# Performance work log

Measured on AMD Instinct MI355X. Metric: run time of the kernel, lower is better.

The kernel has to match this reference:

```python
import jax, jax.numpy as jnp
import numpy as np

HIDDEN = 2048
N_HEADS = 16
HEAD_DIM = HIDDEN // N_HEADS
MAX_POS = 4096
ROPE_THETA = 10000.0
B, S = 2, 4096


def rotate_half(x):
    d = x.shape[-1] // 2
    return jnp.concatenate([-x[..., d:], x[..., :d]], axis=-1)


def make_rope_cache(seq_len, dim, base):
    inv_freq = 1.0 / (base ** (np.arange(0, dim, 2, dtype=np.float32) / dim))
    t = np.arange(seq_len, dtype=np.float32)
    freqs = np.einsum('i,j->ij', t, inv_freq)
    emb = np.concatenate([freqs, freqs], axis=-1)
    return jnp.asarray(np.cos(emb)), jnp.asarray(np.sin(emb))


def setup_inputs() -> dict:
    key = jax.random.key(0)
    k1, k2, k3, k4, k5, k6 = jax.random.split(key, 6)
    hidden_states = jax.random.normal(k1, (B, S, HIDDEN), dtype=jnp.float32)
    # causal additive mask [B,1,S,S]
    causal = jnp.where(jnp.tril(jnp.ones((S, S), dtype=bool)), 0.0, -1e9).astype(jnp.float32)
    attention_mask = jnp.broadcast_to(causal[None, None], (B, 1, S, S))
    position_ids = jnp.broadcast_to(jnp.arange(S, dtype=jnp.int64)[None], (B, S))
    scale = 0.02
    Wq = jax.random.normal(k2, (HIDDEN, HIDDEN), dtype=jnp.float32) * scale
    Wk = jax.random.normal(k3, (HIDDEN, HIDDEN), dtype=jnp.float32) * scale
    Wv = jax.random.normal(k4, (HIDDEN, HIDDEN), dtype=jnp.float32) * scale
    Wo = jax.random.normal(k5, (HIDDEN, HIDDEN), dtype=jnp.float32) * scale
    return {"hidden_states": hidden_states, "attention_mask": attention_mask,
            "position_ids": position_ids, "Wq": Wq, "Wk": Wk, "Wv": Wv, "Wo": Wo}


def reference(hidden_states, attention_mask, position_ids, Wq, Wk, Wv, Wo):
    bsz, q_len, _ = hidden_states.shape
    # projections (torch Linear: x @ W.T; here W stored as [in,out] -> x @ W)
    q = (hidden_states @ Wq).reshape(bsz, q_len, N_HEADS, HEAD_DIM).transpose(0, 2, 1, 3)
    k = (hidden_states @ Wk).reshape(bsz, q_len, N_HEADS, HEAD_DIM).transpose(0, 2, 1, 3)
    v = (hidden_states @ Wv).reshape(bsz, q_len, N_HEADS, HEAD_DIM).transpose(0, 2, 1, 3)
    cos_c, sin_c = make_rope_cache(q_len, HEAD_DIM, ROPE_THETA)
    cos = cos_c[position_ids][:, None]  # [B,1,S,Dh]
    sin = sin_c[position_ids][:, None]
    q = q * cos + rotate_half(q) * sin
    k = k * cos + rotate_half(k) * sin
    scores = jnp.einsum('bhqd,bhkd->bhqk', q, k) / jnp.sqrt(jnp.float32(HEAD_DIM))
    scores = scores + attention_mask
    probs = jax.nn.softmax(scores.astype(jnp.float32), axis=-1).astype(q.dtype)
    attn = jnp.einsum('bhqk,bhkd->bhqd', probs, v)
    attn = attn.transpose(0, 2, 1, 3).reshape(bsz, q_len, HIDDEN)
    return attn @ Wo
```

## Files before the change

### kernel.cpp

```cpp
#include <hip/hip_runtime.h>

#define HID 2048
#define NHEADS 16
#define DHEAD 128
#define BB 2
#define SS 4096
#define MTOT (BB * SS)

typedef __attribute__((ext_vector_type(8))) short short8;
typedef __attribute__((ext_vector_type(8))) unsigned short ushort8;
typedef __attribute__((ext_vector_type(4))) float floatx4;
typedef __attribute__((ext_vector_type(16))) float floatx16;

static __device__ __forceinline__ ushort f2bf(float f) {
  unsigned x = __float_as_uint(f);
  return (ushort)((x + 0x7fffu + ((x >> 16) & 1u)) >> 16);
}
static __device__ __forceinline__ float bf2f(ushort u) {
  return __uint_as_float(((unsigned)u) << 16);
}
static __device__ __forceinline__ unsigned cvtpk_bf16(float lo, float hi) {
  unsigned r;
  asm("v_cvt_pk_bf16_f32 %0, %1, %2" : "=v"(r) : "v"(lo), "v"(hi));
  return r;
}
static __device__ __forceinline__ void pl32swap(unsigned& a, unsigned& b) {
  asm volatile("v_permlane32_swap_b32 %0, %1" : "+v"(a), "+v"(b));
}
static __device__ __forceinline__ floatx16 fz16() {
  floatx16 z;
#pragma unroll
  for (int i = 0; i < 16; i++) z[i] = 0.f;
  return z;
}

#define GL16(g, l)                                                   \
  __builtin_amdgcn_global_load_lds(                                  \
      (const __attribute__((address_space(1))) unsigned int*)(g),    \
      (__attribute__((address_space(3))) unsigned int*)(l), 16, 0, 0)

__global__ __launch_bounds__(256) void k_prep(const float* __restrict__ X,
                                              ushort* __restrict__ Xb,
                                              const float* __restrict__ Wq,
                                              const float* __restrict__ Wk,
                                              const float* __restrict__ Wv,
                                              const float* __restrict__ Wo,
                                              ushort* __restrict__ Wqt,
                                              ushort* __restrict__ Wkt,
                                              ushort* __restrict__ Wvt,
                                              ushort* __restrict__ Wot,
                                              float* __restrict__ cosT,
                                              float* __restrict__ sinT) {
  __shared__ float tile[64][65];
  int id = blockIdx.x, t = threadIdx.x;
  if (id < 2048) {
    int i = id * 256 + t;
    const int n4 = MTOT * HID / 4, stride = 2048 * 256;
    for (; i < n4; i += stride) {
      float4 v = reinterpret_cast<const float4*>(X)[i];
      ushort4 u;
      u.x = f2bf(v.x); u.y = f2bf(v.y); u.z = f2bf(v.z); u.w = f2bf(v.w);
      reinterpret_cast<ushort4*>(Xb)[i] = u;
    }
  } else if (id < 6144) {
    int w = (id - 2048) >> 10;
    int bid = (id - 2048) & 1023;
    const float* W = (w == 0) ? Wq : (w == 1) ? Wk : (w == 2) ? Wv : Wo;
    ushort* Wt = (w == 0) ? Wqt : (w == 1) ? Wkt : (w == 2) ? Wvt : Wot;
    int n0 = (bid & 31) * 64, k0 = (bid >> 5) * 64;
#pragma unroll
    for (int i = 0; i < 16; i++) {
      int idx = t + i * 256, r = idx >> 6, c = idx & 63;
      tile[r][c] = W[(size_t)(k0 + r) * HID + n0 + c];
    }
    __syncthreads();
#pragma unroll
    for (int i = 0; i < 16; i++) {
      int idx = t + i * 256, r = idx >> 6, c = idx & 63;
      Wt[(size_t)(n0 + r) * HID + k0 + c] = f2bf(tile[c][r]);
    }
  } else {
    int idx = (id - 6144) * 256 + t;
    int pos = idx >> 6, j = idx & 63;
    float inv = powf(10000.0f, -(float)(2 * j) * (1.0f / 128.0f));
    float a = (float)pos * inv;
    cosT[idx] = cosf(a);
    sinT[idx] = sinf(a);
  }
}

__global__ void k_rope(ushort* __restrict__ Q, ushort* __restrict__ Kb,
                       const float* __restrict__ cosT, const float* __restrict__ sinT) {
  const float kSc = 0.12751742f;
  int idx = blockIdx.x * 256 + threadIdx.x;
  int j8 = (idx & 7) * 8;
  int hh = (idx >> 3) & (NHEADS - 1);
  int srow = idx >> 7;
  int pos = srow & (SS - 1);
  float4 c0 = *reinterpret_cast<const float4*>(&cosT[pos * 64 + j8]);
  float4 c1 = *reinterpret_cast<const float4*>(&cosT[pos * 64 + j8 + 4]);
  float4 s0 = *reinterpret_cast<const float4*>(&sinT[pos * 64 + j8]);
  float4 s1 = *reinterpret_cast<const float4*>(&sinT[pos * 64 + j8 + 4]);
  float cc[8] = {c0.x, c0.y, c0.z, c0.w, c1.x, c1.y, c1.z, c1.w};
  float ss[8] = {s0.x, s0.y, s0.z, s0.w, s1.x, s1.y, s1.z, s1.w};
  size_t base = (size_t)srow * HID + hh * DHEAD + j8;
  ushort8 qa = *reinterpret_cast<ushort8*>(&Q[base]);
  ushort8 qb = *reinterpret_cast<ushort8*>(&Q[base + 64]);
  ushort8 ka = *reinterpret_cast<ushort8*>(&Kb[base]);
  ushort8 kb = *reinterpret_cast<ushort8*>(&Kb[base + 64]);
  ushort8 o1, o2, o3, o4;
#pragma unroll
  for (int i = 0; i < 8; i++) {
    float a1 = bf2f(qa[i]), a2 = bf2f(qb[i]);
    o1[i] = f2bf((a1 * cc[i] - a2 * ss[i]) * kSc);
    o2[i] = f2bf((a2 * cc[i] + a1 * ss[i]) * kSc);
    float b1 = bf2f(ka[i]), b2 = bf2f(kb[i]);
    o3[i] = f2bf(b1 * cc[i] - b2 * ss[i]);
    o4[i] = f2bf(b2 * cc[i] + b1 * ss[i]);
  }
  *reinterpret_cast<ushort8*>(&Q[base]) = o1;
  *reinterpret_cast<ushort8*>(&Q[base + 64]) = o2;
  *reinterpret_cast<ushort8*>(&Kb[base]) = o3;
  *reinterpret_cast<ushort8*>(&Kb[base + 64]) = o4;
}

template <int OUT_BF16, int DUAL>
__global__ __launch_bounds__(512, 2) void k_gemm8(const ushort* __restrict__ A,
                                                  const ushort* __restrict__ Bt,
                                                  void* __restrict__ Cp,
                                                  const ushort* __restrict__ Bt2,
                                                  void* __restrict__ Cp2,
                                                  int Mr, int Nc, int Kd) {
  __shared__ ushort As[3][256 * 32];
  __shared__ ushort Bs[3][256 * 32];
  int t = threadIdx.x;
  int lane = t & 63, wid = t >> 6;
  int lrow = lane & 15, lk = lane >> 4;
  int wr = wid >> 2, wc = wid & 3;

  int id = blockIdx.x;
  if (DUAL && id >= 256) {
    Bt = Bt2;
    Cp = Cp2;
    id -= 256;
  }
  int nbx = Nc >> 8;
  int swz = (id & 7) * 32 + (id >> 3);
  int m0 = (swz / nbx) << 8, n0 = (swz % nbx) << 8;

  floatx4 acc[8][4];
#pragma unroll
  for (int i = 0; i < 8; i++)
#pragma unroll
    for (int j = 0; j < 4; j++) acc[i][j] = (floatx4){0.f, 0.f, 0.f, 0.f};

  int arow = t >> 2;
  int acol = (((t & 3) ^ (arow & 3)) << 3);
  const ushort* gA = A + (size_t)(m0 + arow) * Kd + acol;
  const ushort* gB = Bt + (size_t)(n0 + arow) * Kd + acol;

  auto STAGE = [&](int buf, int kt) {
    const ushort* a = gA + kt * 32;
    const ushort* bq = gB + kt * 32;
    GL16(a, (char*)As + buf * 16384 + t * 16);
    GL16(a + (size_t)128 * Kd, (char*)As + buf * 16384 + t * 16 + 8192);
    GL16(bq, (char*)Bs + buf * 16384 + t * 16);
    GL16(bq + (size_t)128 * Kd, (char*)Bs + buf * 16384 + t * 16 + 8192);
  };

  STAGE(0, 0);
  STAGE(1, 1);

  int nk = Kd >> 5;
  for (int tK = 0; tK < nk; ++tK) {
    if (tK + 1 < nk)
      asm volatile("s_waitcnt vmcnt(4)" ::: "memory");
    else
      asm volatile("s_waitcnt vmcnt(0)" ::: "memory");
    __builtin_amdgcn_s_barrier();
    asm volatile("" ::: "memory");
    int buf = tK % 3;
    const char* Ab_ = (const char*)As + buf * 16384;
    const char* Bb_ = (const char*)Bs + buf * 16384;
    short8 af[8], bfr[4];
#pragma unroll
    for (int fm = 0; fm < 8; fm++) {
      int row = wr * 128 + fm * 16 + lrow;
      af[fm] = *reinterpret_cast<const short8*>(
          Ab_ + ((row * 64 + lk * 16) ^ ((row & 3) << 4)));
    }
#pragma unroll
    for (int fn = 0; fn < 4; fn++) {
      int row = wc * 64 + fn * 16 + lrow;
      bfr[fn] = *reinterpret_cast<const short8*>(
          Bb_ + ((row * 64 + lk * 16) ^ ((row & 3) << 4)));
    }
    if (tK + 2 < nk) STAGE((tK + 2) % 3, tK + 2);
    __builtin_amdgcn_s_setprio(1);
#pragma unroll
    for (int fm = 0; fm < 8; fm++)
#pragma unroll
      for (int fn = 0; fn < 4; fn++)
        acc[fm][fn] = __builtin_amdgcn_mfma_f32_16x16x32_bf16(af[fm], bfr[fn],
                                                              acc[fm][fn], 0, 0, 0);
    __builtin_amdgcn_s_setprio(0);
  }

#pragma unroll
  for (int am = 0; am < 8; am++)
#pragma unroll
    for (int an = 0; an < 4; an++)
#pragma unroll
      for (int r = 0; r < 4; r++) {
        int m = m0 + wr * 128 + am * 16 + lk * 4 + r;
        int n = n0 + wc * 64 + an * 16 + lrow;
        if (OUT_BF16)
          ((ushort*)Cp)[(size_t)m * Nc + n] = f2bf(acc[am][an][r]);
        else
          ((float*)Cp)[(size_t)m * Nc + n] = acc[am][an][r];
      }
}

__global__ __launch_bounds__(512, 2) void k_fattn(const ushort* __restrict__ Qg,
                                                  const ushort* __restrict__ Kg,
                                                  const ushort* __restrict__ Vt2,
                                                  ushort* __restrict__ Og) {
  __shared__ ushort Ks[2][64 * 128];
  __shared__ ushort Vs[2][128 * 64];
  int t = threadIdx.x, lane = t & 63, wid = t >> 6;
  int l31 = lane & 31, hi = lane >> 5;
  int id = blockIdx.x;
  int qt = 15 - (id >> 5);
  int h = id & 15, b = (id >> 4) & 1;

  auto STAGE = [&](int buf, int kt) {
    int kv0 = kt * 64;
    const ushort* Kbase = Kg + (size_t)(b * SS + kv0) * HID + h * DHEAD;
    const ushort* Vbase = Vt2 + (size_t)(h * DHEAD) * MTOT + b * SS + kv0;
#pragma unroll
    for (int i = 0; i < 2; i++) {
      int L = t + i * 512;
      int row = L >> 4, cr = L & 15;
      GL16(Kbase + (size_t)row * HID + ((cr ^ (row & 15)) << 3),
           (char*)Ks + buf * 16384 + L * 16);
    }
#pragma unroll
    for (int i = 0; i < 2; i++) {
      int L = t + i * 512;
      int row = L >> 3, cr = L & 7;
      GL16(Vbase + (size_t)row * MTOT + ((cr ^ (row & 7)) << 3),
           (char*)Vs + buf * 16384 + L * 16);
    }
  };

  int q0 = qt * 256;
  int wq0 = q0 + wid * 32;
  int qlane = wq0 + l31;

  short8 qf[8];
  {
    const ushort* qb = Qg + (size_t)(b * SS + qlane) * HID + h * DHEAD + hi * 8;
#pragma unroll
    for (int ks = 0; ks < 8; ks++)
      qf[ks] = *reinterpret_cast<const short8*>(qb + ks * 16);
  }

  floatx16 accO[4];
#pragma unroll
  for (int db = 0; db < 4; db++) accO[db] = fz16();
  float mrow = -1e30f, lsum = 0.f;

  int nkt = (qt + 1) * 4;
  STAGE(0, 0);

  for (int kt = 0; kt < nkt; kt++) {
    int cur = kt & 1;
    int kv0 = kt * 64;
    bool pre = (kt + 1 < nkt);
    if (pre) {
      STAGE(cur ^ 1, kt + 1);
      asm volatile("s_waitcnt vmcnt(4)" ::: "memory");
    } else {
      asm volatile("s_waitcnt vmcnt(0)" ::: "memory");
    }
    __builtin_amdgcn_s_barrier();
    asm volatile("" ::: "memory");

    if (kv0 <= wq0 + 31) {
      const char* Kb_ = (const char*)Ks + cur * 16384;
      floatx16 accS[2];
      accS[0] = fz16(); accS[1] = fz16();
      __builtin_amdgcn_s_setprio(1);
#pragma unroll
      for (int ks = 0; ks < 8; ks++) {
#pragma unroll
        for (int kvb = 0; kvb < 2; kvb++) {
          int row = kvb * 32 + l31;
          int byte_ = (row * 256 + ks * 32 + hi * 16) ^ ((row & 15) << 4);
          short8 kf = *reinterpret_cast<const short8*>(Kb_ + byte_);
          accS[kvb] = __builtin_amdgcn_mfma_f32_32x32x16_bf16(kf, qf[ks], accS[kvb], 0, 0, 0);
        }
      }
      __builtin_amdgcn_s_setprio(0);

      if (kv0 + 63 > wq0) {
        int kvbase = kv0 + hi * 4;
#pragma unroll
        for (int kvb = 0; kvb < 2; kvb++)
#pragma unroll
          for (int r = 0; r < 16; r++) {
            int kvi = kvbase + kvb * 32 + (r & 3) + 8 * (r >> 2);
            if (kvi > qlane) accS[kvb][r] = -1e30f;
          }
      }

      float mA = -1e30f, mB = -1e30f, mC = -1e30f, mD = -1e30f;
#pragma unroll
      for (int r = 0; r < 16; r += 4) {
        mA = fmaxf(mA, fmaxf(accS[0][r], accS[1][r]));
        mB = fmaxf(mB, fmaxf(accS[0][r + 1], accS[1][r + 1]));
        mC = fmaxf(mC, fmaxf(accS[0][r + 2], accS[1][r + 2]));
        mD = fmaxf(mD, fmaxf(accS[0][r + 3], accS[1][r + 3]));
      }
      float mx = fmaxf(fmaxf(mA, mB), fmaxf(mC, mD));
      mx = fmaxf(mx, __shfl_xor(mx, 32));
      if (!__all(mx <= mrow + 8.0f)) {
        float mnew = fmaxf(mrow, mx);
        float corr = exp2f(mrow - mnew);
        mrow = mnew;
        lsum *= corr;
#pragma unroll
        for (int db = 0; db < 4; db++)
#pragma unroll
          for (int r = 0; r < 16; r++) accO[db][r] *= corr;
      }

      float sA = 0.f, sB = 0.f, sC = 0.f, sD = 0.f;
#pragma unroll
      for (int kvb = 0; kvb < 2; kvb++)
#pragma unroll
        for (int r = 0; r < 16; r += 4) {
          float p0 = exp2f(accS[kvb][r] - mrow);
          float p1 = exp2f(accS[kvb][r + 1] - mrow);
          float p2 = exp2f(accS[kvb][r + 2] - mrow);
          float p3 = exp2f(accS[kvb][r + 3] - mrow);
          accS[kvb][r] = p0; accS[kvb][r + 1] = p1;
          accS[kvb][r + 2] = p2; accS[kvb][r + 3] = p3;
          sA += p0; sB += p1; sC += p2; sD += p3;
        }
      lsum += ((sA + sB) + (sC + sD));

      const char* Vb_ = (const char*)Vs + cur * 16384;
#pragma unroll
      for (int ks = 0; ks < 4; ks++) {
        int kvb = ks >> 1, tt = ks & 1;
        unsigned w0 = cvtpk_bf16(accS[kvb][8 * tt + 0], accS[kvb][8 * tt + 1]);
        unsigned w2 = cvtpk_bf16(accS[kvb][8 * tt + 4], accS[kvb][8 * tt + 5]);
        pl32swap(w0, w2);
        unsigned w1 = cvtpk_bf16(accS[kvb][8 * tt + 2], accS[kvb][8 * tt + 3]);
        unsigned w3 = cvtpk_bf16(accS[kvb][8 * tt + 6], accS[kvb][8 * tt + 7]);
        pl32swap(w1, w3);
        union { unsigned u[4]; short8 v; } pf;
        pf.u[0] = w0; pf.u[1] = w1; pf.u[2] = w2; pf.u[3] = w3;
        __builtin_amdgcn_s_setprio(1);
#pragma unroll
        for (int db = 0; db < 4; db++) {
          int row = db * 32 + l31;
          int byte_ = (row * 128 + ks * 32 + hi * 16) ^ ((row & 7) << 4);
          short8 vf = *reinterpret_cast<const short8*>(Vb_ + byte_);
          accO[db] = __builtin_amdgcn_mfma_f32_32x32x16_bf16(vf, pf.v, accO[db], 0, 0, 0);
        }
        __builtin_amdgcn_s_setprio(0);
      }
    }
    asm volatile("" ::: "memory");
    __builtin_amdgcn_s_barrier();
    asm volatile("" ::: "memory");
  }

  float lt = lsum + __shfl_xor(lsum, 32);
  float inv = 1.0f / lt;
  char* sb = ((wid < 4) ? (char*)Ks : (char*)Vs) + (wid & 3) * 8192;
#pragma unroll
  for (int db = 0; db < 4; db++)
#pragma unroll
    for (int r = 0; r < 16; r += 2) {
      int d = db * 32 + (r & 3) + 8 * (r >> 2) + hi * 4;
      unsigned w = cvtpk_bf16(accO[db][r] * inv, accO[db][r + 1] * inv);
      int byte_ = (l31 * 256 + d * 2) ^ ((l31 & 15) << 4);
      *reinterpret_cast<unsigned*>(sb + byte_) = w;
    }
#pragma unroll
  for (int i = 0; i < 8; i++) {
    int row = i * 4 + (lane >> 4);
    int byte_ = (row * 256 + (lane & 15) * 16) ^ ((row & 15) << 4);
    ushort8 ov = *reinterpret_cast<const ushort8*>(sb + byte_);
    *reinterpret_cast<ushort8*>(Og + (size_t)(b * SS + wq0 + row) * HID + h * DHEAD +
                                (lane & 15) * 8) = ov;
  }
}

extern "C" void kernel_launch(void* const* d_in, const int* in_sizes, int n_in,
                              void* d_out, int out_size, void* d_ws, size_t ws_size,
                              hipStream_t stream) {
  const float* X = (const float*)d_in[0];
  const float* Wq = (const float*)d_in[3];
  const float* Wk = (const float*)d_in[4];
  const float* Wv = (const float*)d_in[5];
  const float* Wo = (const float*)d_in[6];
  float* out = (float*)d_out;

  char* p = (char*)d_ws;
  const size_t szXb = (size_t)MTOT * HID * 2;
  const size_t szW = (size_t)HID * HID * 2;
  ushort* Xb = (ushort*)p;  p += szXb;
  ushort* Wqt = (ushort*)p; p += szW;
  ushort* Wkt = (ushort*)p; p += szW;
  ushort* Wvt = (ushort*)p; p += szW;
  ushort* Wot = (ushort*)p; p += szW;
  ushort* Qb = (ushort*)p;  p += szXb;
  ushort* Kb = (ushort*)p;  p += szXb;
  ushort* Vt2 = (ushort*)p; p += szXb;
  ushort* Ab = (ushort*)p;  p += szXb;
  float* cosT = (float*)p;  p += (size_t)SS * 64 * 4;
  float* sinT = (float*)p;  p += (size_t)SS * 64 * 4;

  k_prep<<<7168, 256, 0, stream>>>(X, Xb, Wq, Wk, Wv, Wo, Wqt, Wkt, Wvt, Wot,
                                   cosT, sinT);

  k_gemm8<1, 1><<<512, 512, 0, stream>>>(Xb, Wqt, Qb, Wkt, Kb, MTOT, HID, HID);
  k_gemm8<1, 0><<<256, 512, 0, stream>>>(Wvt, Xb, Vt2, nullptr, nullptr, HID, MTOT, HID);

  k_rope<<<MTOT * NHEADS * 8 / 256, 256, 0, stream>>>(Qb, Kb, cosT, sinT);

  k_fattn<<<512, 512, 0, stream>>>(Qb, Kb, Vt2, Ab);

  k_gemm8<0, 0><<<256, 512, 0, stream>>>(Ab, Wot, out, nullptr, nullptr, MTOT, HID, HID);
}
```

Baseline: 518.4 us.

## Fuse RoPE into V-projection launch and retile flash attention to 128-query blocks

The separate RoPE kernel is folded into the V-projection GEMM launch as extra blocks, so the elementwise rotation runs alongside the GEMM instead of as its own launch. Flash attention is retiled from 256-query, 8-wave blocks with 64-key tiles to 128-query, 4-wave blocks with 32-key tiles. That doubles the grid and aims for better load balance across the causal triangle and higher occupancy. The trade-off is more barriers and staging steps per unit of work, less MFMA work per iteration, and RoPE blocks that carry the GEMM's large shared-memory footprint.

```diff
diff --git a/kernel.cpp b/kernel.cpp
--- a/kernel.cpp
+++ b/kernel.cpp
@@ -89,41 +89,6 @@
   }
 }
 
-__global__ void k_rope(ushort* __restrict__ Q, ushort* __restrict__ Kb,
-                       const float* __restrict__ cosT, const float* __restrict__ sinT) {
-  const float kSc = 0.12751742f;
-  int idx = blockIdx.x * 256 + threadIdx.x;
-  int j8 = (idx & 7) * 8;
-  int hh = (idx >> 3) & (NHEADS - 1);
-  int srow = idx >> 7;
-  int pos = srow & (SS - 1);
-  float4 c0 = *reinterpret_cast<const float4*>(&cosT[pos * 64 + j8]);
-  float4 c1 = *reinterpret_cast<const float4*>(&cosT[pos * 64 + j8 + 4]);
-  float4 s0 = *reinterpret_cast<const float4*>(&sinT[pos * 64 + j8]);
-  float4 s1 = *reinterpret_cast<const float4*>(&sinT[pos * 64 + j8 + 4]);
-  float cc[8] = {c0.x, c0.y, c0.z, c0.w, c1.x, c1.y, c1.z, c1.w};
-  float ss[8] = {s0.x, s0.y, s0.z, s0.w, s1.x, s1.y, s1.z, s1.w};
-  size_t base = (size_t)srow * HID + hh * DHEAD + j8;
-  ushort8 qa = *reinterpret_cast<ushort8*>(&Q[base]);
-  ushort8 qb = *reinterpret_cast<ushort8*>(&Q[base + 64]);
-  ushort8 ka = *reinterpret_cast<ushort8*>(&Kb[base]);
-  ushort8 kb = *reinterpret_cast<ushort8*>(&Kb[base + 64]);
-  ushort8 o1, o2, o3, o4;
-#pragma unroll
-  for (int i = 0; i < 8; i++) {
-    float a1 = bf2f(qa[i]), a2 = bf2f(qb[i]);
-    o1[i] = f2bf((a1 * cc[i] - a2 * ss[i]) * kSc);
-    o2[i] = f2bf((a2 * cc[i] + a1 * ss[i]) * kSc);
-    float b1 = bf2f(ka[i]), b2 = bf2f(kb[i]);
-    o3[i] = f2bf(b1 * cc[i] - b2 * ss[i]);
-    o4[i] = f2bf(b2 * cc[i] + b1 * ss[i]);
-  }
-  *reinterpret_cast<ushort8*>(&Q[base]) = o1;
-  *reinterpret_cast<ushort8*>(&Q[base + 64]) = o2;
-  *reinterpret_cast<ushort8*>(&Kb[base]) = o3;
-  *reinterpret_cast<ushort8*>(&Kb[base + 64]) = o4;
-}
-
 template <int OUT_BF16, int DUAL>
 __global__ __launch_bounds__(512, 2) void k_gemm8(const ushort* __restrict__ A,
                                                   const ushort* __restrict__ Bt,
@@ -221,39 +186,163 @@
       }
 }
 
-__global__ __launch_bounds__(512, 2) void k_fattn(const ushort* __restrict__ Qg,
+__global__ __launch_bounds__(512, 2) void k_gvrope(const ushort* __restrict__ A,
+                                                   const ushort* __restrict__ Bt,
+                                                   ushort* __restrict__ Cp,
+                                                   ushort* __restrict__ Q,
+                                                   ushort* __restrict__ Kb,
+                                                   const float* __restrict__ cosT,
+                                                   const float* __restrict__ sinT) {
+  __shared__ ushort As[3][256 * 32];
+  __shared__ ushort Bs[3][256 * 32];
+  int t = threadIdx.x;
+  if (blockIdx.x >= 256) {
+    const float kSc = 0.12751742f;
+    int idx = (blockIdx.x - 256) * 512 + t;
+    int j8 = (idx & 7) * 8;
+    int hh = (idx >> 3) & (NHEADS - 1);
+    int srow = idx >> 7;
+    int pos = srow & (SS - 1);
+    float4 c0 = *reinterpret_cast<const float4*>(&cosT[pos * 64 + j8]);
+    float4 c1 = *reinterpret_cast<const float4*>(&cosT[pos * 64 + j8 + 4]);
+    float4 s0 = *reinterpret_cast<const float4*>(&sinT[pos * 64 + j8]);
+    float4 s1 = *reinterpret_cast<const float4*>(&sinT[pos * 64 + j8 + 4]);
+    float cc[8] = {c0.x, c0.y, c0.z, c0.w, c1.x, c1.y, c1.z, c1.w};
+    float ss[8] = {s0.x, s0.y, s0.z, s0.w, s1.x, s1.y, s1.z, s1.w};
+    size_t base = (size_t)srow * HID + hh * DHEAD + j8;
+    ushort8 qa = *reinterpret_cast<ushort8*>(&Q[base]);
+    ushort8 qb = *reinterpret_cast<ushort8*>(&Q[base + 64]);
+    ushort8 ka = *reinterpret_cast<ushort8*>(&Kb[base]);
+    ushort8 kb = *reinterpret_cast<ushort8*>(&Kb[base + 64]);
+    ushort8 o1, o2, o3, o4;
+#pragma unroll
+    for (int i = 0; i < 8; i++) {
+      float a1 = bf2f(qa[i]), a2 = bf2f(qb[i]);
+      o1[i] = f2bf((a1 * cc[i] - a2 * ss[i]) * kSc);
+      o2[i] = f2bf((a2 * cc[i] + a1 * ss[i]) * kSc);
+      float b1 = bf2f(ka[i]), b2 = bf2f(kb[i]);
+      o3[i] = f2bf(b1 * cc[i] - b2 * ss[i]);
+      o4[i] = f2bf(b2 * cc[i] + b1 * ss[i]);
+    }
+    *reinterpret_cast<ushort8*>(&Q[base]) = o1;
+    *reinterpret_cast<ushort8*>(&Q[base + 64]) = o2;
+    *reinterpret_cast<ushort8*>(&Kb[base]) = o3;
+    *reinterpret_cast<ushort8*>(&Kb[base + 64]) = o4;
+    return;
+  }
+
+  const int Nc = MTOT, Kd = HID;
+  int lane = t & 63, wid = t >> 6;
+  int lrow = lane & 15, lk = lane >> 4;
+  int wr = wid >> 2, wc = wid & 3;
+  int id = blockIdx.x;
+  int nbx = Nc >> 8;
+  int swz = (id & 7) * 32 + (id >> 3);
+  int m0 = (swz / nbx) << 8, n0 = (swz % nbx) << 8;
+
+  floatx4 acc[8][4];
+#pragma unroll
+  for (int i = 0; i < 8; i++)
+#pragma unroll
+    for (int j = 0; j < 4; j++) acc[i][j] = (floatx4){0.f, 0.f, 0.f, 0.f};
+
+  int arow = t >> 2;
+  int acol = (((t & 3) ^ (arow & 3)) << 3);
+  const ushort* gA = A + (size_t)(m0 + arow) * Kd + acol;
+  const ushort* gB = Bt + (size_t)(n0 + arow) * Kd + acol;
+
+  auto STAGE = [&](int buf, int kt) {
+    const ushort* a = gA + kt * 32;
+    const ushort* bq = gB + kt * 32;
+    GL16(a, (char*)As + buf * 16384 + t * 16);
+    GL16(a + (size_t)128 * Kd, (char*)As + buf * 16384 + t * 16 + 8192);
+    GL16(bq, (char*)Bs + buf * 16384 + t * 16);
+    GL16(bq + (size_t)128 * Kd, (char*)Bs + buf * 16384 + t * 16 + 8192);
+  };
+
+  STAGE(0, 0);
+  STAGE(1, 1);
+
+  int nk = Kd >> 5;
+  for (int tK = 0; tK < nk; ++tK) {
+    if (tK + 1 < nk)
+      asm volatile("s_waitcnt vmcnt(4)" ::: "memory");
+    else
+      asm volatile("s_waitcnt vmcnt(0)" ::: "memory");
+    __builtin_amdgcn_s_barrier();
+    asm volatile("" ::: "memory");
+    int buf = tK % 3;
+    const char* Ab_ = (const char*)As + buf * 16384;
+    const char* Bb_ = (const char*)Bs + buf * 16384;
+    short8 af[8], bfr[4];
+#pragma unroll
+    for (int fm = 0; fm < 8; fm++) {
+      int row = wr * 128 + fm * 16 + lrow;
+      af[fm] = *reinterpret_cast<const short8*>(
+          Ab_ + ((row * 64 + lk * 16) ^ ((row & 3) << 4)));
+    }
+#pragma unroll
+    for (int fn = 0; fn < 4; fn++) {
+      int row = wc * 64 + fn * 16 + lrow;
+      bfr[fn] = *reinterpret_cast<const short8*>(
+          Bb_ + ((row * 64 + lk * 16) ^ ((row & 3) << 4)));
+    }
+    if (tK + 2 < nk) STAGE((tK + 2) % 3, tK + 2);
+    __builtin_amdgcn_s_setprio(1);
+#pragma unroll
+    for (int fm = 0; fm < 8; fm++)
+#pragma unroll
+      for (int fn = 0; fn < 4; fn++)
+        acc[fm][fn] = __builtin_amdgcn_mfma_f32_16x16x32_bf16(af[fm], bfr[fn],
+                                                              acc[fm][fn], 0, 0, 0);
+    __builtin_amdgcn_s_setprio(0);
+  }
+
+#pragma unroll
+  for (int am = 0; am < 8; am++)
+#pragma unroll
+    for (int an = 0; an < 4; an++)
+#pragma unroll
+      for (int r = 0; r < 4; r++) {
+        int m = m0 + wr * 128 + am * 16 + lk * 4 + r;
+        int n = n0 + wc * 64 + an * 16 + lrow;
+        Cp[(size_t)m * Nc + n] = f2bf(acc[am][an][r]);
+      }
+}
+
+__global__ __launch_bounds__(256, 4) void k_fattn(const ushort* __restrict__ Qg,
                                                   const ushort* __restrict__ Kg,
                                                   const ushort* __restrict__ Vt2,
                                                   ushort* __restrict__ Og) {
-  __shared__ ushort Ks[2][64 * 128];
-  __shared__ ushort Vs[2][128 * 64];
+  __shared__ ushort Ks[2][32 * 128];
+  __shared__ ushort Vs[2][128 * 32];
   int t = threadIdx.x, lane = t & 63, wid = t >> 6;
   int l31 = lane & 31, hi = lane >> 5;
   int id = blockIdx.x;
-  int qt = 15 - (id >> 5);
+  int qt = 31 - (id >> 5);
   int h = id & 15, b = (id >> 4) & 1;
 
   auto STAGE = [&](int buf, int kt) {
-    int kv0 = kt * 64;
+    int kv0 = kt * 32;
     const ushort* Kbase = Kg + (size_t)(b * SS + kv0) * HID + h * DHEAD;
     const ushort* Vbase = Vt2 + (size_t)(h * DHEAD) * MTOT + b * SS + kv0;
 #pragma unroll
     for (int i = 0; i < 2; i++) {
-      int L = t + i * 512;
+      int L = t + i * 256;
       int row = L >> 4, cr = L & 15;
       GL16(Kbase + (size_t)row * HID + ((cr ^ (row & 15)) << 3),
-           (char*)Ks + buf * 16384 + L * 16);
+           (char*)Ks + buf * 8192 + L * 16);
     }
 #pragma unroll
     for (int i = 0; i < 2; i++) {
-      int L = t + i * 512;
-      int row = L >> 3, cr = L & 7;
-      GL16(Vbase + (size_t)row * MTOT + ((cr ^ (row & 7)) << 3),
-           (char*)Vs + buf * 16384 + L * 16);
+      int L = t + i * 256;
+      int row = L >> 2, cr = L & 3;
+      GL16(Vbase + (size_t)row * MTOT + ((cr ^ (row & 3)) << 3),
+           (char*)Vs + buf * 8192 + L * 16);
     }
   };
 
-  int q0 = qt * 256;
+  int q0 = qt * 128;
   int wq0 = q0 + wid * 32;
   int qlane = wq0 + l31;
 
@@ -275,7 +364,7 @@
 
   for (int kt = 0; kt < nkt; kt++) {
     int cur = kt & 1;
-    int kv0 = kt * 64;
+    int kv0 = kt * 32;
     bool pre = (kt + 1 < nkt);
     if (pre) {
       STAGE(cur ^ 1, kt + 1);
@@ -287,40 +376,34 @@
     asm volatile("" ::: "memory");
 
     if (kv0 <= wq0 + 31) {
-      const char* Kb_ = (const char*)Ks + cur * 16384;
-      floatx16 accS[2];
-      accS[0] = fz16(); accS[1] = fz16();
+      const char* Kb_ = (const char*)Ks + cur * 8192;
+      floatx16 accS = fz16();
       __builtin_amdgcn_s_setprio(1);
 #pragma unroll
       for (int ks = 0; ks < 8; ks++) {
-#pragma unroll
-        for (int kvb = 0; kvb < 2; kvb++) {
-          int row = kvb * 32 + l31;
-          int byte_ = (row * 256 + ks * 32 + hi * 16) ^ ((row & 15) << 4);
-          short8 kf = *reinterpret_cast<const short8*>(Kb_ + byte_);
-          accS[kvb] = __builtin_amdgcn_mfma_f32_32x32x16_bf16(kf, qf[ks], accS[kvb], 0, 0, 0);
+        int row = l31;
+        int byte_ = (row * 256 + ks * 32 + hi * 16) ^ ((row & 15) << 4);
+        short8 kf = *reinterpret_cast<const short8*>(Kb_ + byte_);
+        accS = __builtin_amdgcn_mfma_f32_32x32x16_bf16(kf, qf[ks], accS, 0, 0, 0);
+      }
+      __builtin_amdgcn_s_setprio(0);
+
+      if (kv0 + 31 > wq0) {
+        int kvbase = kv0 + hi * 4;
+#pragma unroll
+        for (int r = 0; r < 16; r++) {
+          int kvi = kvbase + (r & 3) + 8 * (r >> 2);
+          if (kvi > qlane) accS[r] = -1e30f;
         }
       }
-      __builtin_amdgcn_s_setprio(0);
-
-      if (kv0 + 63 > wq0) {
-        int kvbase = kv0 + hi * 4;
-#pragma unroll
-        for (int kvb = 0; kvb < 2; kvb++)
-#pragma unroll
-          for (int r = 0; r < 16; r++) {
-            int kvi = kvbase + kvb * 32 + (r & 3) + 8 * (r >> 2);
-            if (kvi > qlane) accS[kvb][r] = -1e30f;
-          }
-      }
 
       float mA = -1e30f, mB = -1e30f, mC = -1e30f, mD = -1e30f;
 #pragma unroll
       for (int r = 0; r < 16; r += 4) {
-        mA = fmaxf(mA, fmaxf(accS[0][r], accS[1][r]));
-        mB = fmaxf(mB, fmaxf(accS[0][r + 1], accS[1][r + 1]));
-        mC = fmaxf(mC, fmaxf(accS[0][r + 2], accS[1][r + 2]));
-        mD = fmaxf(mD, fmaxf(accS[0][r + 3], accS[1][r + 3]));
+        mA = fmaxf(mA, accS[r]);
+        mB = fmaxf(mB, accS[r + 1]);
+        mC = fmaxf(mC, accS[r + 2]);
+        mD = fmaxf(mD, accS[r + 3]);
       }
       float mx = fmaxf(fmaxf(mA, mB), fmaxf(mC, mD));
       mx = fmaxf(mx, __shfl_xor(mx, 32));
@@ -337,28 +420,25 @@
 
       float sA = 0.f, sB = 0.f, sC = 0.f, sD = 0.f;
 #pragma unroll
-      for (int kvb = 0; kvb < 2; kvb++)
-#pragma unroll
-        for (int r = 0; r < 16; r += 4) {
-          float p0 = exp2f(accS[kvb][r] - mrow);
-          float p1 = exp2f(accS[kvb][r + 1] - mrow);
-          float p2 = exp2f(accS[kvb][r + 2] - mrow);
-          float p3 = exp2f(accS[kvb][r + 3] - mrow);
-          accS[kvb][r] = p0; accS[kvb][r + 1] = p1;
-          accS[kvb][r + 2] = p2; accS[kvb][r + 3] = p3;
-          sA += p0; sB += p1; sC += p2; sD += p3;
-        }
+      for (int r = 0; r < 16; r += 4) {
+        float p0 = exp2f(accS[r] - mrow);
+        float p1 = exp2f(accS[r + 1] - mrow);
+        float p2 = exp2f(accS[r + 2] - mrow);
+        float p3 = exp2f(accS[r + 3] - mrow);
+        accS[r] = p0; accS[r + 1] = p1; accS[r + 2] = p2; accS[r + 3] = p3;
+        sA += p0; sB += p1; sC += p2; sD += p3;
+      }
       lsum += ((sA + sB) + (sC + sD));
 
-      const char* Vb_ = (const char*)Vs + cur * 16384;
-#pragma unroll
-      for (int ks = 0; ks < 4; ks++) {
-        int kvb = ks >> 1, tt = ks & 1;
-        unsigned w0 = cvtpk_bf16(accS[kvb][8 * tt + 0], accS[kvb][8 * tt + 1]);
-        unsigned w2 = cvtpk_bf16(accS[kvb][8 * tt + 4], accS[kvb][8 * tt + 5]);
+      const char* Vb_ = (const char*)Vs + cur * 8192;
+#pragma unroll
+      for (int ks = 0; ks < 2; ks++) {
+        int tt = ks;
+        unsigned w0 = cvtpk_bf16(accS[8 * tt + 0], accS[8 * tt + 1]);
+        unsigned w2 = cvtpk_bf16(accS[8 * tt + 4], accS[8 * tt + 5]);
         pl32swap(w0, w2);
-        unsigned w1 = cvtpk_bf16(accS[kvb][8 * tt + 2], accS[kvb][8 * tt + 3]);
-        unsigned w3 = cvtpk_bf16(accS[kvb][8 * tt + 6], accS[kvb][8 * tt + 7]);
+        unsigned w1 = cvtpk_bf16(accS[8 * tt + 2], accS[8 * tt + 3]);
+        unsigned w3 = cvtpk_bf16(accS[8 * tt + 6], accS[8 * tt + 7]);
         pl32swap(w1, w3);
         union { unsigned u[4]; short8 v; } pf;
         pf.u[0] = w0; pf.u[1] = w1; pf.u[2] = w2; pf.u[3] = w3;
@@ -366,7 +446,7 @@
 #pragma unroll
         for (int db = 0; db < 4; db++) {
           int row = db * 32 + l31;
-          int byte_ = (row * 128 + ks * 32 + hi * 16) ^ ((row & 7) << 4);
+          int byte_ = (row * 64 + ks * 32 + hi * 16) ^ ((row & 3) << 4);
           short8 vf = *reinterpret_cast<const short8*>(Vb_ + byte_);
           accO[db] = __builtin_amdgcn_mfma_f32_32x32x16_bf16(vf, pf.v, accO[db], 0, 0, 0);
         }
@@ -380,7 +460,7 @@
 
   float lt = lsum + __shfl_xor(lsum, 32);
   float inv = 1.0f / lt;
-  char* sb = ((wid < 4) ? (char*)Ks : (char*)Vs) + (wid & 3) * 8192;
+  char* sb = ((wid < 2) ? (char*)Ks : (char*)Vs) + (wid & 1) * 8192;
 #pragma unroll
   for (int db = 0; db < 4; db++)
 #pragma unroll
@@ -429,11 +509,9 @@
                                    cosT, sinT);
 
   k_gemm8<1, 1><<<512, 512, 0, stream>>>(Xb, Wqt, Qb, Wkt, Kb, MTOT, HID, HID);
-  k_gemm8<1, 0><<<256, 512, 0, stream>>>(Wvt, Xb, Vt2, nullptr, nullptr, HID, MTOT, HID);
-
-  k_rope<<<MTOT * NHEADS * 8 / 256, 256, 0, stream>>>(Qb, Kb, cosT, sinT);
-
-  k_fattn<<<512, 512, 0, stream>>>(Qb, Kb, Vt2, Ab);
+  k_gvrope<<<2304, 512, 0, stream>>>(Wvt, Xb, Vt2, Qb, Kb, cosT, sinT);
+
+  k_fattn<<<1024, 256, 0, stream>>>(Qb, Kb, Vt2, Ab);
 
   k_gemm8<0, 0><<<256, 512, 0, stream>>>(Ab, Wot, out, nullptr, nullptr, MTOT, HID, HID);
 }
```

After: 796.2 us. +53.6%, slower.
